# Kernel optimization log

Hardware: AMD Instinct MI355X
Metric: run time of the kernel (lower is better)

The kernel has to match this reference:

```python
import jax, jax.numpy as jnp
import numpy as np
from jax import lax

B, N, C = 16, 16384, 90      # batch, anchors, classes
K = 100                      # per-class pre-NMS top-k
MAX_DET = 100                # final detections per image
IOU_THR = 0.5
SCORE_THR = 0.05


def setup_inputs() -> dict:
    key = jax.random.key(0)
    k1, k2, k3, k4 = jax.random.split(key, 4)
    box_encodings = jax.random.normal(k1, (B, N, 4), dtype=jnp.float32) * 0.5
    class_logits = jax.random.normal(k2, (B, N, C), dtype=jnp.float32) * 2.0 - 3.0
    # anchors as [ymin,xmin,ymax,xmax] in normalized coords
    centers = jax.random.uniform(k3, (N, 2), dtype=jnp.float32)             # (cy,cx)
    sizes = jax.random.uniform(k4, (N, 2), dtype=jnp.float32, minval=0.05, maxval=0.3)
    anchors = jnp.concatenate([centers - sizes / 2, centers + sizes / 2], axis=-1)
    return {"box_encodings": box_encodings, "class_logits": class_logits, "anchors": anchors}


def decode_boxes(enc, anchors):
    ymin, xmin, ymax, xmax = [anchors[:, i] for i in range(4)]
    ha, wa = ymax - ymin, xmax - xmin
    cya, cxa = (ymin + ymax) / 2, (xmin + xmax) / 2
    ty, tx, th, tw = enc[..., 0] / 10.0, enc[..., 1] / 10.0, enc[..., 2] / 5.0, enc[..., 3] / 5.0
    cy = ty * ha + cya
    cx = tx * wa + cxa
    h = jnp.exp(th) * ha
    w = jnp.exp(tw) * wa
    boxes = jnp.stack([cy - h / 2, cx - w / 2, cy + h / 2, cx + w / 2], axis=-1)
    return jnp.clip(boxes, 0.0, 1.0)  # [..., N, 4]


def pairwise_iou(b):  # b: [K,4]
    area = jnp.maximum(b[:, 2] - b[:, 0], 0) * jnp.maximum(b[:, 3] - b[:, 1], 0)
    iy = jnp.maximum(jnp.minimum(b[:, None, 2], b[None, :, 2]) - jnp.maximum(b[:, None, 0], b[None, :, 0]), 0)
    ix = jnp.maximum(jnp.minimum(b[:, None, 3], b[None, :, 3]) - jnp.maximum(b[:, None, 1], b[None, :, 1]), 0)
    inter = iy * ix
    union = area[:, None] + area[None, :] - inter
    return inter / jnp.maximum(union, 1e-8)


def nms_one_class(boxes, scores_c):  # boxes [N,4], scores_c [N]
    vals, idx = lax.top_k(scores_c, K)           # sorted descending
    bk = boxes[idx]                               # [K,4]
    iou = pairwise_iou(bk)                        # [K,K]
    def step(keep, i):
        supp = jnp.any(keep & (iou[i] >= IOU_THR))
        ki = (vals[i] > SCORE_THR) & (~supp)
        return keep.at[i].set(ki), None
    keep, _ = lax.scan(step, jnp.zeros((K,), bool), jnp.arange(K))
    return bk, vals * keep                        # suppressed -> score 0


def postprocess_one(boxes, scores):  # boxes [N,4], scores [N,C]
    bx_ck, sc_ck = jax.vmap(nms_one_class, in_axes=(None, 1))(boxes, scores)  # [C,K,4],[C,K]
    cls_ck = jnp.broadcast_to(jnp.arange(C, dtype=jnp.float32)[:, None], (C, K))
    sc_f = sc_ck.reshape(-1)
    fsc, fidx = lax.top_k(sc_f, MAX_DET)
    fbx = bx_ck.reshape(-1, 4)[fidx]
    fcl = cls_ck.reshape(-1)[fidx]
    return jnp.concatenate([fbx, fcl[:, None], fsc[:, None]], axis=-1)  # [MAX_DET, 6]


def reference(box_encodings, class_logits, anchors):
    boxes = decode_boxes(box_encodings, anchors)       # [B,N,4]
    scores = jax.nn.sigmoid(class_logits)              # [B,N,C]
    combined = jax.vmap(postprocess_one)(boxes, scores)  # [B,MAX_DET,6] = boxes|class|score
    return combined
```

## Files before the change

### kernel.cpp

```cpp
#include <hip/hip_runtime.h>
#include <stdint.h>
#include <math.h>

#define B_ 16
#define NN 16384
#define C_ 90
#define KSEL 100
#define MAXD 100
#define MFLAT (C_ * KSEL)
#define NPAIR 128
#define ZKEY 0x80000000u


__device__ __forceinline__ uint32_t fkey(float f) {
  uint32_t u = __float_as_uint(f);
  return (u & 0x80000000u) ? ~u : (u | 0x80000000u);
}
__device__ __forceinline__ float keyinv(uint32_t k) {
  uint32_t u = (k & 0x80000000u) ? (k & 0x7FFFFFFFu) : ~k;
  return __uint_as_float(u);
}

__device__ __forceinline__ uint32_t blockSum512(uint32_t v, uint32_t* red, uint32_t* s_total) {
  int tid = threadIdx.x;
#pragma unroll
  for (int o = 32; o > 0; o >>= 1) v += __shfl_down(v, o, 64);
  if ((tid & 63) == 0) red[tid >> 6] = v;
  __syncthreads();
  if (tid == 0) {
    uint32_t s = 0;
#pragma unroll
    for (int i = 0; i < 8; ++i) s += red[i];
    *s_total = s;
  }
  __syncthreads();
  return *s_total;
}

__global__ __launch_bounds__(256) void transpose_key16_kernel(const float* __restrict__ logits,
                                                              uint16_t* __restrict__ keys16T) {
  __shared__ uint32_t tile[128 * 91];
  int b = blockIdx.y;
  int n0 = blockIdx.x * 128;
  const float4* src4 = reinterpret_cast<const float4*>(logits + ((size_t)b * NN + n0) * C_);
  for (int p = threadIdx.x; p < 2880; p += 256) {
    float4 v = src4[p];
    int e = p * 4;
    float vv[4] = {v.x, v.y, v.z, v.w};
#pragma unroll
    for (int j = 0; j < 4; ++j) {
      int ee = e + j;
      tile[(ee / C_) * 91 + (ee % C_)] = fkey(vv[j]);
    }
  }
  __syncthreads();
  uint16_t* dstb = keys16T + (size_t)b * C_ * NN + n0;
  for (int q = threadIdx.x; q < C_ * 16; q += 256) {
    int c = q >> 4, g = q & 15;
    int nn2 = g * 8;
    uint4 o;
    o.x = (tile[(nn2 + 0) * 91 + c] >> 16) | (tile[(nn2 + 1) * 91 + c] & 0xFFFF0000u);
    o.y = (tile[(nn2 + 2) * 91 + c] >> 16) | (tile[(nn2 + 3) * 91 + c] & 0xFFFF0000u);
    o.z = (tile[(nn2 + 4) * 91 + c] >> 16) | (tile[(nn2 + 5) * 91 + c] & 0xFFFF0000u);
    o.w = (tile[(nn2 + 6) * 91 + c] >> 16) | (tile[(nn2 + 7) * 91 + c] & 0xFFFF0000u);
    reinterpret_cast<uint4*>(dstb + (size_t)c * NN)[g] = o;
  }
}

template <int TR>
__global__ __launch_bounds__(512, 8) void select_kernel(
    const uint16_t* __restrict__ keys16T,
    const float* __restrict__ logits,
    uint32_t* __restrict__ candPacked,
    uint32_t* __restrict__ candCount) {
  __shared__ uint32_t hist[2048];
  __shared__ uint32_t sc[512];
  __shared__ uint32_t ws8[64];
  __shared__ int s_bsel;
  __shared__ uint32_t s_Sincl, s_Sexcl;
  __shared__ uint32_t red[8];
  __shared__ uint32_t s_total;
  __shared__ uint32_t s_cnt;

  const int c = blockIdx.x, b = blockIdx.y;
  const int tid = threadIdx.x;

  uint32_t keyw[16];
  if (TR) {
    const uint4* src4 = reinterpret_cast<const uint4*>(keys16T + ((size_t)b * C_ + c) * NN);
#pragma unroll
    for (int q = 0; q < 4; ++q) {
      uint4 kv = src4[q * 512 + tid];
      keyw[4 * q + 0] = kv.x; keyw[4 * q + 1] = kv.y;
      keyw[4 * q + 2] = kv.z; keyw[4 * q + 3] = kv.w;
    }
  } else {
    const float* src = logits + (size_t)b * NN * C_ + c;
#pragma unroll
    for (int m = 0; m < 16; ++m) {
      uint32_t i0 = (uint32_t)((((m >> 2) * 512 + tid) * 8) + ((m & 3) * 2));
      uint32_t klo = fkey(src[(size_t)i0 * C_]) >> 16;
      uint32_t khi = fkey(src[(size_t)(i0 + 1) * C_]) >> 16;
      keyw[m] = klo | (khi << 16);
    }
  }

  reinterpret_cast<uint4*>(hist)[tid] = make_uint4(0u, 0u, 0u, 0u);
  __syncthreads();
#pragma unroll
  for (int m = 0; m < 16; ++m) {
    uint32_t w = keyw[m];
    atomicAdd(&hist[(w & 0xFFFFu) >> 5], 1u);
    atomicAdd(&hist[w >> 21], 1u);
  }
  __syncthreads();

  uint32_t m_above = 0;
  uint32_t need = 100u;
  uint32_t cut16 = 0;
  int found = 0;
  int tiepath = 0;
  uint32_t V16 = 0, Texact = NN - 1;

  {
    uint32_t h0 = hist[4 * tid], h1 = hist[4 * tid + 1];
    uint32_t h2 = hist[4 * tid + 2], h3 = hist[4 * tid + 3];
    sc[tid] = h0 + h1 + h2 + h3;
    if (tid == 0) s_bsel = -1;
    __syncthreads();
    if (tid < 64) {
      uint32_t w = 0;
      int base = tid * 8;
#pragma unroll
      for (int i = 0; i < 8; ++i) w += sc[base + i];
#pragma unroll
      for (int off = 1; off < 64; off <<= 1) {
        uint32_t v = __shfl_down(w, off, 64);
        if (tid + off < 64) w += v;
      }
      ws8[tid] = w;
    }
    __syncthreads();
    {
      int g = tid >> 3;
      uint32_t above = (g < 63) ? ws8[g + 1] : 0u;
      for (int j = (g << 3) + 7; j > tid; --j) above += sc[j];
      uint32_t run = above;
      int best = -1;
      uint32_t bi = 0, be = 0;
      uint32_t hh[4] = {h0, h1, h2, h3};
#pragma unroll
      for (int p = 3; p >= 0; --p) {
        uint32_t h = hh[p];
        run += h;
        if (best < 0 && run >= need) { best = 4 * tid + p; bi = run; be = run - h; }
      }
      if (best >= 0) atomicMax(&s_bsel, best);
      __syncthreads();
      if (best >= 0 && best == s_bsel) { s_Sincl = bi; s_Sexcl = be; }
    }
    __syncthreads();

    uint32_t bsel = (uint32_t)s_bsel;
    uint32_t Sincl = s_Sincl, Sexcl = s_Sexcl;
    if (Sincl <= (uint32_t)NPAIR) {
      cut16 = bsel << 5;
      found = 1;
    } else {
      m_above = Sexcl;
      need = 100u - m_above;
      __syncthreads();
      if (tid < 8) reinterpret_cast<uint4*>(hist)[tid] = make_uint4(0u, 0u, 0u, 0u);
      __syncthreads();
#pragma unroll
      for (int m = 0; m < 16; ++m) {
        uint32_t w = keyw[m];
        uint32_t klo = w & 0xFFFFu, khi = w >> 16;
        if ((klo >> 5) == bsel) atomicAdd(&hist[klo & 31u], 1u);
        if ((khi >> 5) == bsel) atomicAdd(&hist[khi & 31u], 1u);
      }
      __syncthreads();
      uint32_t run = 0;
      int b1 = -1;
      uint32_t Si = 0, Se = 0;
      for (int p = 31; p >= 0; --p) {
        uint32_t h = hist[p];
        run += h;
        if (b1 < 0 && run >= need) { b1 = p; Si = run; Se = run - h; }
      }
      uint32_t cutv = (bsel << 5) | (uint32_t)b1;
      if (m_above + Si <= (uint32_t)NPAIR) {
        cut16 = cutv;
        found = 1;
      } else {
        tiepath = 1;
        V16 = cutv;
        m_above += Se;
        uint32_t r = 100u - m_above;
        uint32_t lo2 = 0, hi2 = NN - 1;
        while (lo2 < hi2) {
          uint32_t mid2 = lo2 + ((hi2 - lo2) >> 1);
          uint32_t cnt = 0;
#pragma unroll
          for (int m = 0; m < 16; ++m) {
            uint32_t w = keyw[m];
            uint32_t i0 = (uint32_t)((((m >> 2) * 512 + tid) * 8) + ((m & 3) * 2));
            cnt += ((w & 0xFFFFu) == V16 && i0 <= mid2) ? 1u : 0u;
            cnt += ((w >> 16) == V16 && (i0 + 1) <= mid2) ? 1u : 0u;
          }
          uint32_t tot = blockSum512(cnt, red, &s_total);
          if (tot >= r) hi2 = mid2; else lo2 = mid2 + 1;
        }
        Texact = lo2;
      }
    }
  }

  if (tid == 0) s_cnt = 0;
  __syncthreads();
  uint32_t* outp = candPacked + (size_t)(b * C_ + c) * NPAIR;
#pragma unroll
  for (int m = 0; m < 16; ++m) {
    uint32_t w = keyw[m];
    uint32_t i0 = (uint32_t)((((m >> 2) * 512 + tid) * 8) + ((m & 3) * 2));
    uint32_t klo = w & 0xFFFFu, khi = w >> 16;
    bool t0 = tiepath ? (klo > V16 || (klo == V16 && i0 <= Texact)) : (klo >= cut16);
    bool t1 = tiepath ? (khi > V16 || (khi == V16 && (i0 + 1) <= Texact)) : (khi >= cut16);
    if (t0) {
      uint32_t p = atomicAdd(&s_cnt, 1u);
      if (p < (uint32_t)NPAIR) outp[p] = (klo << 16) | i0;
    }
    if (t1) {
      uint32_t p = atomicAdd(&s_cnt, 1u);
      if (p < (uint32_t)NPAIR) outp[p] = (khi << 16) | (i0 + 1);
    }
  }
  __syncthreads();
  if (tid == 0) candCount[b * C_ + c] = (s_cnt > (uint32_t)NPAIR) ? (uint32_t)NPAIR : s_cnt;
}

__global__ __launch_bounds__(256, 8) void sort_nms_kernel(
    const uint32_t* __restrict__ candPacked,
    const uint32_t* __restrict__ candCount,
    const float* __restrict__ logits,
    const float* __restrict__ enc,
    const float* __restrict__ anchors,
    float* __restrict__ candBox,
    float* __restrict__ candScore) {
  __shared__ unsigned long long ck[NPAIR];
  __shared__ float p_box[NPAIR][5];
  __shared__ float p_area[NPAIR];
  __shared__ float p_val[NPAIR];
  __shared__ unsigned long long M[NPAIR][2];
  __shared__ uint32_t s_sl[KSEL];
  __shared__ unsigned long long s_keepw[2];

  const int c = blockIdx.x, b = blockIdx.y;
  const int tid = threadIdx.x;
  const int bc = b * C_ + c;
  const uint32_t cnt = candCount[bc];

  float ry1 = 0, rx1 = 0, ry2 = 0, rx2 = 0, rar = 0;

  if (tid < NPAIR) {
    int s = tid;
    uint32_t v = candPacked[(size_t)bc * NPAIR + s];
    int n = (s < (int)cnt) ? (int)(v & 0x3FFFu) : 0;
    float x = logits[((size_t)b * NN + n) * C_ + c];
    float sv = 1.0f / (1.0f + expf(-x));
    p_val[s] = sv;
    unsigned long long ckv = 0ull;
    if (s < (int)cnt)
      ckv = ((unsigned long long)fkey(sv) << 32) |
            (unsigned long long)((((uint32_t)(NN - 1 - n)) << 7) | (uint32_t)s);
    ck[s] = ckv;
  } else {
    int s = tid - NPAIR;
    uint32_t v = candPacked[(size_t)bc * NPAIR + s];
    int n = (s < (int)cnt) ? (int)(v & 0x3FFFu) : 0;
    float4 e = reinterpret_cast<const float4*>(enc)[(size_t)b * NN + n];
    float4 a = reinterpret_cast<const float4*>(anchors)[n];
    float ha = a.z - a.x, wa = a.w - a.y;
    float cya = (a.x + a.z) * 0.5f, cxa = (a.y + a.w) * 0.5f;
    float cy = (e.x / 10.0f) * ha + cya;
    float cx = (e.y / 10.0f) * wa + cxa;
    float h = expf(e.z / 5.0f) * ha;
    float w = expf(e.w / 5.0f) * wa;
    ry1 = fminf(fmaxf(cy - h * 0.5f, 0.0f), 1.0f);
    rx1 = fminf(fmaxf(cx - w * 0.5f, 0.0f), 1.0f);
    ry2 = fminf(fmaxf(cy + h * 0.5f, 0.0f), 1.0f);
    rx2 = fminf(fmaxf(cx + w * 0.5f, 0.0f), 1.0f);
    rar = fmaxf(ry2 - ry1, 0.0f) * fmaxf(rx2 - rx1, 0.0f);
    p_box[s][0] = ry1; p_box[s][1] = rx1; p_box[s][2] = ry2; p_box[s][3] = rx2;
    p_area[s] = rar;
  }
  __syncthreads();

  unsigned long long m0 = 0ull, m1 = 0ull;
  int step = 0;
  for (int kk = 2; kk <= 128; kk <<= 1) {
    for (int j = kk >> 1; j > 0; j >>= 1) {
      if (tid < NPAIR) {
        int ixj = tid ^ j;
        if (ixj > tid) {
          unsigned long long aa = ck[tid], bb2 = ck[ixj];
          if ((aa < bb2) == ((tid & kk) == 0)) { ck[tid] = bb2; ck[ixj] = aa; }
        }
      } else {
        int c0 = step * 5;
#pragma unroll
        for (int qq = 0; qq < 5; ++qq) {
          int q = c0 + qq;
          if (q < NPAIR) {
            float iy1 = p_box[q][0], ix1 = p_box[q][1];
            float iy2 = p_box[q][2], ix2 = p_box[q][3];
            float ta = fmaxf(fminf(iy2, ry2) - fmaxf(iy1, ry1), 0.0f) *
                       fmaxf(fminf(ix2, rx2) - fmaxf(ix1, rx1), 0.0f);
            float un = fmaxf(p_area[q] + rar - ta, 1e-8f);
            bool hit = (ta / un >= 0.5f);
            if (q < 64) m0 |= (unsigned long long)hit << q;
            else        m1 |= (unsigned long long)hit << (q - 64);
          }
        }
      }
      ++step;
      __syncthreads();
    }
  }
  if (tid >= NPAIR) {
    int s = tid - NPAIR;
    M[s][0] = m0; M[s][1] = m1;
  }
  __syncthreads();
  if (tid < KSEL) {
    uint32_t sl = (uint32_t)ck[tid] & 127u;
    s_sl[tid] = sl | ((p_val[sl] > 0.05f) ? 256u : 0u);
  }
  __syncthreads();

  if (tid < 64) {
    unsigned long long supp0 = 0, supp1 = 0, k0 = 0, k1 = 0;
#pragma unroll 4
    for (int j = 0; j < KSEL; ++j) {
      uint32_t e = s_sl[j];
      int sl = (int)(e & 127u);
      unsigned long long r0 = M[sl][0], r1 = M[sl][1];
      bool suppd = (sl < 64) ? ((supp0 >> sl) & 1ull) : ((supp1 >> (sl - 64)) & 1ull);
      bool pass = (e & 256u) && !suppd;
      if (pass) {
        supp0 |= r0; supp1 |= r1;
        if (j < 64) k0 |= 1ull << j; else k1 |= 1ull << (j - 64);
      }
    }
    if (tid == 0) { s_keepw[0] = k0; s_keepw[1] = k1; }
  }
  __syncthreads();

  if (tid < KSEL) {
    unsigned long long keyv = ck[tid];
    int slot = (int)((uint32_t)keyv & 127u);
    bool kept = (tid < 64) ? ((s_keepw[0] >> tid) & 1ull)
                           : ((s_keepw[1] >> (tid - 64)) & 1ull);
    size_t base = (size_t)bc * KSEL + tid;
    candScore[base] = kept ? keyinv((uint32_t)(keyv >> 32)) : 0.0f;
    float* cb = candBox + base * 4;
    cb[0] = p_box[slot][0]; cb[1] = p_box[slot][1];
    cb[2] = p_box[slot][2]; cb[3] = p_box[slot][3];
  }
}

#define FT_NT 512
#define FT_SLOTS 18
#define FT_NW 8
__global__ __launch_bounds__(FT_NT) void final_topk_kernel(
    const float* __restrict__ candScore,
    const float* __restrict__ candBox,
    float* __restrict__ out) {
  __shared__ uint32_t skey[FT_NT * FT_SLOTS];
  __shared__ uint32_t hist[FT_NW * 2048];
  __shared__ uint32_t sc[512];
  __shared__ uint32_t ws8[64];
  __shared__ int s_bsel;
  __shared__ uint32_t s_Sincl, s_Sexcl;
  __shared__ uint32_t red[8];
  __shared__ uint32_t s_total;
  __shared__ uint32_t s_cnt;
  __shared__ unsigned long long ck[128];

  int b = blockIdx.x, tid = threadIdx.x;
  const int wid = tid >> 6;
  const float* src = candScore + (size_t)b * MFLAT;

  uint32_t nzc = 0;
  for (int q = 0; q < FT_SLOTS; ++q) {
    int idx = q * FT_NT + tid;
    uint32_t k = (idx < MFLAT) ? fkey(src[idx]) : 0u;
    skey[idx] = k;
    nzc += (k > ZKEY) ? 1u : 0u;
  }
  __syncthreads();
  uint32_t nz = blockSum512(nzc, red, &s_total);

  uint32_t cutHi = 0, m_above = 0, cut32 = 0;
  int found = 0, tiepath = 0;
  uint32_t V32 = 0, Texact = (uint32_t)(MFLAT - 1);
  uint32_t tie_r = 0;

  if (nz < 100u) {
    tiepath = 1;
    V32 = ZKEY;
    tie_r = 100u - nz;
  } else {
    for (int lvl = 0; lvl < 3; ++lvl) {
      const int shiftLo = (lvl == 0) ? 21 : (lvl == 1) ? 10 : 0;
      const uint32_t mask = (lvl == 2) ? 0x3FFu : 0x7FFu;
      const int nbits = (lvl == 2) ? 10 : 11;

      for (int i = tid; i < FT_NW * 512; i += FT_NT)
        reinterpret_cast<uint4*>(hist)[i] = make_uint4(0u, 0u, 0u, 0u);
      __syncthreads();
      uint32_t* myh = hist + wid * 2048;
      for (int q = 0; q < FT_SLOTS; ++q) {
        uint32_t k = skey[q * FT_NT + tid];
        bool in = (k > ZKEY) && ((lvl == 0) ? true : ((k >> (shiftLo + nbits)) == cutHi));
        if (in) atomicAdd(&myh[(k >> shiftLo) & mask], 1u);
      }
      __syncthreads();

      const uint32_t need = 100u - m_above;

      uint32_t h0 = 0, h1 = 0, h2 = 0, h3 = 0;
#pragma unroll
      for (int w = 0; w < FT_NW; ++w) {
        uint4 a = *reinterpret_cast<const uint4*>(hist + w * 2048 + 4 * tid);
        h0 += a.x; h1 += a.y; h2 += a.z; h3 += a.w;
      }
      sc[tid] = h0 + h1 + h2 + h3;
      if (tid == 0) s_bsel = -1;
      __syncthreads();
      if (tid < 64) {
        uint32_t w = 0;
        int base = tid * 8;
#pragma unroll
        for (int i = 0; i < 8; ++i) w += sc[base + i];
#pragma unroll
        for (int off = 1; off < 64; off <<= 1) {
          uint32_t v = __shfl_down(w, off, 64);
          if (tid + off < 64) w += v;
        }
        ws8[tid] = w;
      }
      __syncthreads();
      {
        int g = tid >> 3;
        uint32_t above = (g < 63) ? ws8[g + 1] : 0u;
        for (int j = (g << 3) + 7; j > tid; --j) above += sc[j];
        uint32_t run = above;
        int best = -1;
        uint32_t bi = 0, be = 0;
        uint32_t hh[4] = {h0, h1, h2, h3};
#pragma unroll
        for (int p = 3; p >= 0; --p) {
          uint32_t h = hh[p];
          run += h;
          if (best < 0 && run >= need) { best = 4 * tid + p; bi = run; be = run - h; }
        }
        if (best >= 0) atomicMax(&s_bsel, best);
        __syncthreads();
        if (best >= 0 && best == s_bsel) { s_Sincl = bi; s_Sexcl = be; }
      }
      __syncthreads();

      uint32_t bsel = (uint32_t)s_bsel;
      cutHi = (cutHi << nbits) | bsel;
      if (m_above + s_Sincl <= 128u) {
        cut32 = cutHi << shiftLo;
        found = 1;
        break;
      }
      m_above += s_Sexcl;
      __syncthreads();
    }

    if (!found) {
      tiepath = 1;
      V32 = cutHi;
      tie_r = 100u - m_above;
    }
  }

  if (tiepath) {
    uint32_t lo2 = 0, hi2 = (uint32_t)(MFLAT - 1);
    while (lo2 < hi2) {
      uint32_t mid2 = lo2 + ((hi2 - lo2) >> 1);
      uint32_t cnt = 0;
      for (int q = 0; q < FT_SLOTS; ++q) {
        uint32_t idx = (uint32_t)(q * FT_NT + tid);
        cnt += (skey[idx] == V32 && idx <= mid2) ? 1u : 0u;
      }
      uint32_t tot = blockSum512(cnt, red, &s_total);
      if (tot >= tie_r) hi2 = mid2; else lo2 = mid2 + 1;
    }
    Texact = lo2;
  }

  if (tid == 0) s_cnt = 0;
  __syncthreads();
  for (int q = 0; q < FT_SLOTS; ++q) {
    uint32_t idx = (uint32_t)(q * FT_NT + tid);
    uint32_t k = skey[idx];
    bool take = tiepath ? (k > V32 || (k == V32 && idx <= Texact))
                        : (k > ZKEY && k >= cut32);
    if (take) {
      uint32_t p = atomicAdd(&s_cnt, 1u);
      if (p < 128u)
        ck[p] = ((unsigned long long)k << 32) | (unsigned long long)(~idx);
    }
  }
  __syncthreads();
  if (tid < 128 && (uint32_t)tid >= s_cnt) ck[tid] = 0ull;
  __syncthreads();

  for (int kk = 2; kk <= 128; kk <<= 1) {
    for (int j = kk >> 1; j > 0; j >>= 1) {
      if (tid < 128) {
        int ixj = tid ^ j;
        if (ixj > tid) {
          unsigned long long a = ck[tid], bb = ck[ixj];
          if ((a < bb) == ((tid & kk) == 0)) { ck[tid] = bb; ck[ixj] = a; }
        }
      }
      __syncthreads();
    }
  }

  if (tid < MAXD) {
    unsigned long long keyv = ck[tid];
    int f = (int)(~(uint32_t)(keyv & 0xFFFFFFFFull));
    int c = f / KSEL;
    float sc2 = keyinv((uint32_t)(keyv >> 32));
    const float* cb = candBox + ((size_t)b * MFLAT + f) * 4;
    float* o = out + ((size_t)b * MAXD + tid) * 6;
    o[0] = cb[0]; o[1] = cb[1]; o[2] = cb[2]; o[3] = cb[3];
    o[4] = (float)c; o[5] = sc2;
  }
}

extern "C" void kernel_launch(void* const* d_in, const int* in_sizes, int n_in,
                              void* d_out, int out_size, void* d_ws, size_t ws_size,
                              hipStream_t stream) {
  const float* enc = (const float*)d_in[0];
  const float* logits = (const float*)d_in[1];
  const float* anchors = (const float*)d_in[2];
  float* out = (float*)d_out;
  char* ws = (char*)d_ws;

  size_t off = 0;
  float* candBox = (float*)(ws + off);   off += (size_t)B_ * C_ * KSEL * 4 * sizeof(float);
  float* candScore = (float*)(ws + off); off += (size_t)B_ * C_ * KSEL * sizeof(float);
  uint32_t* candPacked = (uint32_t*)(ws + off);
  off += (size_t)B_ * C_ * NPAIR * sizeof(uint32_t);
  uint32_t* candCount = (uint32_t*)(ws + off); off += (size_t)B_ * C_ * sizeof(uint32_t);
  off = (off + 255) & ~(size_t)255;
  uint16_t* keys16T = (uint16_t*)(ws + off);
  size_t needT = off + (size_t)B_ * C_ * NN * sizeof(uint16_t);
  int transposed = (ws_size >= needT) ? 1 : 0;

  if (transposed) {
    transpose_key16_kernel<<<dim3(NN / 128, B_), 256, 0, stream>>>(logits, keys16T);
    select_kernel<1><<<dim3(C_, B_), 512, 0, stream>>>(keys16T, logits, candPacked, candCount);
  } else {
    select_kernel<0><<<dim3(C_, B_), 512, 0, stream>>>(keys16T, logits, candPacked, candCount);
  }

  sort_nms_kernel<<<dim3(C_, B_), 256, 0, stream>>>(candPacked, candCount, logits,
                                                    enc, anchors, candBox, candScore);

  final_topk_kernel<<<B_, FT_NT, 0, stream>>>(candScore, candBox, out);
}
```

Before: 138.0 us.

## Replace bitonic sort with rank-by-counting and barrier-free IoU mask

Drops the 28-stage shared-memory bitonic sort over 128 candidate keys, where every stage needed a block barrier. Each of the first 128 threads now computes its rank by comparing its key against all others and scatters its slot into s_sl. The other 128 threads build the IoU bitmask in one loop with float4 box loads. Invalid keys are made unique so ranks do not collide. The cost is O(N^2) shared-memory comparisons per thread in exchange for removing about 28 barriers.

Result: faster. 134.7 us, median of 2 (-2.4%).

```diff
diff --git a/kernel.cpp b/kernel.cpp
--- a/kernel.cpp
+++ b/kernel.cpp
@@ -248,11 +248,10 @@
     float* __restrict__ candBox,
     float* __restrict__ candScore) {
   __shared__ unsigned long long ck[NPAIR];
-  __shared__ float p_box[NPAIR][5];
+  __shared__ float p_box[NPAIR][4];
   __shared__ float p_area[NPAIR];
-  __shared__ float p_val[NPAIR];
   __shared__ unsigned long long M[NPAIR][2];
-  __shared__ uint32_t s_sl[KSEL];
+  __shared__ uint32_t s_sl[NPAIR];
   __shared__ unsigned long long s_keepw[2];
 
   const int c = blockIdx.x, b = blockIdx.y;
@@ -260,6 +259,8 @@
   const int bc = b * C_ + c;
   const uint32_t cnt = candCount[bc];
 
+  unsigned long long myKey = 0ull;
+  bool myOk = false;
   float ry1 = 0, rx1 = 0, ry2 = 0, rx2 = 0, rar = 0;
 
   if (tid < NPAIR) {
@@ -268,12 +269,12 @@
     int n = (s < (int)cnt) ? (int)(v & 0x3FFFu) : 0;
     float x = logits[((size_t)b * NN + n) * C_ + c];
     float sv = 1.0f / (1.0f + expf(-x));
-    p_val[s] = sv;
-    unsigned long long ckv = 0ull;
-    if (s < (int)cnt)
-      ckv = ((unsigned long long)fkey(sv) << 32) |
-            (unsigned long long)((((uint32_t)(NN - 1 - n)) << 7) | (uint32_t)s);
-    ck[s] = ckv;
+    myOk = (sv > 0.05f);
+    myKey = (s < (int)cnt)
+        ? (((unsigned long long)fkey(sv) << 32) |
+           (unsigned long long)((((uint32_t)(NN - 1 - n)) << 7) | (uint32_t)s))
+        : (unsigned long long)s;
+    ck[s] = myKey;
   } else {
     int s = tid - NPAIR;
     uint32_t v = candPacked[(size_t)bc * NPAIR + s];
@@ -291,50 +292,32 @@
     ry2 = fminf(fmaxf(cy + h * 0.5f, 0.0f), 1.0f);
     rx2 = fminf(fmaxf(cx + w * 0.5f, 0.0f), 1.0f);
     rar = fmaxf(ry2 - ry1, 0.0f) * fmaxf(rx2 - rx1, 0.0f);
-    p_box[s][0] = ry1; p_box[s][1] = rx1; p_box[s][2] = ry2; p_box[s][3] = rx2;
+    float4* pb = reinterpret_cast<float4*>(p_box[s]);
+    *pb = make_float4(ry1, rx1, ry2, rx2);
     p_area[s] = rar;
   }
   __syncthreads();
 
-  unsigned long long m0 = 0ull, m1 = 0ull;
-  int step = 0;
-  for (int kk = 2; kk <= 128; kk <<= 1) {
-    for (int j = kk >> 1; j > 0; j >>= 1) {
-      if (tid < NPAIR) {
-        int ixj = tid ^ j;
-        if (ixj > tid) {
-          unsigned long long aa = ck[tid], bb2 = ck[ixj];
-          if ((aa < bb2) == ((tid & kk) == 0)) { ck[tid] = bb2; ck[ixj] = aa; }
-        }
-      } else {
-        int c0 = step * 5;
-#pragma unroll
-        for (int qq = 0; qq < 5; ++qq) {
-          int q = c0 + qq;
-          if (q < NPAIR) {
-            float iy1 = p_box[q][0], ix1 = p_box[q][1];
-            float iy2 = p_box[q][2], ix2 = p_box[q][3];
-            float ta = fmaxf(fminf(iy2, ry2) - fmaxf(iy1, ry1), 0.0f) *
-                       fmaxf(fminf(ix2, rx2) - fmaxf(ix1, rx1), 0.0f);
-            float un = fmaxf(p_area[q] + rar - ta, 1e-8f);
-            bool hit = (ta / un >= 0.5f);
-            if (q < 64) m0 |= (unsigned long long)hit << q;
-            else        m1 |= (unsigned long long)hit << (q - 64);
-          }
-        }
-      }
-      ++step;
-      __syncthreads();
-    }
-  }
-  if (tid >= NPAIR) {
+  if (tid < NPAIR) {
+    uint32_t rank = 0;
+#pragma unroll 8
+    for (int j = 0; j < NPAIR; ++j) rank += (ck[j] > myKey) ? 1u : 0u;
+    s_sl[rank] = (uint32_t)tid | (myOk ? 256u : 0u);
+  } else {
     int s = tid - NPAIR;
+    unsigned long long m0 = 0ull, m1 = 0ull;
+#pragma unroll 4
+    for (int q = 0; q < NPAIR; ++q) {
+      float4 bq = *reinterpret_cast<const float4*>(p_box[q]);
+      float aq = p_area[q];
+      float ta = fmaxf(fminf(bq.z, ry2) - fmaxf(bq.x, ry1), 0.0f) *
+                 fmaxf(fminf(bq.w, rx2) - fmaxf(bq.y, rx1), 0.0f);
+      float un = fmaxf(aq + rar - ta, 1e-8f);
+      bool hit = (ta / un >= 0.5f);
+      if (q < 64) m0 |= (unsigned long long)hit << q;
+      else        m1 |= (unsigned long long)hit << (q - 64);
+    }
     M[s][0] = m0; M[s][1] = m1;
-  }
-  __syncthreads();
-  if (tid < KSEL) {
-    uint32_t sl = (uint32_t)ck[tid] & 127u;
-    s_sl[tid] = sl | ((p_val[sl] > 0.05f) ? 256u : 0u);
   }
   __syncthreads();
 
@@ -357,8 +340,8 @@
   __syncthreads();
 
   if (tid < KSEL) {
-    unsigned long long keyv = ck[tid];
-    int slot = (int)((uint32_t)keyv & 127u);
+    int slot = (int)(s_sl[tid] & 127u);
+    unsigned long long keyv = ck[slot];
     bool kept = (tid < 64) ? ((s_keepw[0] >> tid) & 1ull)
                            : ((s_keepw[1] >> (tid - 64)) & 1ull);
     size_t base = (size_t)bc * KSEL + tid;
```
